# Optimization experiments

Hardware: AMD Instinct MI355X
Metric: run time of the kernel (lower is better)

## Reference

```python
import jax, jax.numpy as jnp
import numpy as np

N_NODES = 100000
N_EDGES = 3200000
F_IN, F_HID, F_OUT = 36, 8, 2
NEG_SLOPE = 0.2


def gat_layer(x, src, dst, W, a_src, a_dst, b, num_nodes):
    # Linear transform: [N, F'] 
    h = x @ W
    # Per-node attention logits (heads=1)
    alpha_s = h @ a_src  # [N]
    alpha_d = h @ a_dst  # [N]
    # Edge-wise score: leaky_relu(a_src . h_j + a_dst . h_i) for edge j->i
    e = jax.nn.leaky_relu(alpha_s[src] + alpha_d[dst], negative_slope=NEG_SLOPE)  # [E]
    # Segment softmax over incoming edges of each dst node
    m = jax.ops.segment_max(e, dst, num_segments=num_nodes)  # [N]
    ee = jnp.exp(e - m[dst])
    denom = jax.ops.segment_sum(ee, dst, num_segments=num_nodes)  # [N]
    alpha = ee / denom[dst]  # [E]
    # Scatter-aggregate messages
    out = jax.ops.segment_sum(alpha[:, None] * h[src], dst, num_segments=num_nodes)
    return out + b


def setup_inputs() -> dict:
    key = jax.random.key(0)
    ks = jax.random.split(key, 10)
    x = jax.random.normal(ks[0], (N_NODES, F_IN), dtype=jnp.float32)
    edge_index = jax.random.randint(ks[1], (2, N_EDGES), 0, N_NODES, dtype=jnp.int64)
    s1 = 1.0 / np.sqrt(F_IN)
    s2 = 1.0 / np.sqrt(F_HID)
    W1 = jax.random.uniform(ks[2], (F_IN, F_HID), jnp.float32, -s1, s1)
    a_src1 = jax.random.uniform(ks[3], (F_HID,), jnp.float32, -s2, s2)
    a_dst1 = jax.random.uniform(ks[4], (F_HID,), jnp.float32, -s2, s2)
    b1 = jnp.zeros((F_HID,), jnp.float32)
    W2 = jax.random.uniform(ks[5], (F_HID, F_OUT), jnp.float32, -s2, s2)
    so = 1.0 / np.sqrt(F_OUT)
    a_src2 = jax.random.uniform(ks[6], (F_OUT,), jnp.float32, -so, so)
    a_dst2 = jax.random.uniform(ks[7], (F_OUT,), jnp.float32, -so, so)
    b2 = jnp.zeros((F_OUT,), jnp.float32)
    return {"x": x, "edge_index": edge_index, "W1": W1, "a_src1": a_src1,
            "a_dst1": a_dst1, "b1": b1, "W2": W2, "a_src2": a_src2,
            "a_dst2": a_dst2, "b2": b2}


def reference(x, edge_index, W1, a_src1, a_dst1, b1, W2, a_src2, a_dst2, b2):
    src, dst = edge_index[0], edge_index[1]
    n = x.shape[0]
    h = jax.nn.relu(gat_layer(x, src, dst, W1, a_src1, a_dst1, b1, n))
    # dropout is identity in eval mode
    out = gat_layer(h, src, dst, W2, a_src2, a_dst2, b2, n)
    return jax.nn.log_softmax(out, axis=1)
```

## Files before the change

### kernel.cpp

```cpp
#include <hip/hip_runtime.h>
#include <hip/hip_bf16.h>

#define N_NODES 100000
#define N_EDGES 3200000
#define F_IN 36
#define F_HID 8
#define F_OUT 2
#define NEG_SLOPE 0.2f

#define SHIFT_C 10
#define NCB 98
#define CAPC 36000
#define GSHIFT 6
#define GNPB 64
#define NFINE 1568
#define CAPF 2368
#define NB_PART 512
#define CHUNK 6250
#define BP 512
#define NSLICE 16
#define BP2 256
#define BPG 256

__device__ __forceinline__ int detect_is64(const void* eidx, int* s_flag) {
    if (threadIdx.x < 64) {
        const unsigned int* p = (const unsigned int*)eidx;
        unsigned int v1 = p[2 * threadIdx.x + 1];
        unsigned int v2 = p[2 * (threadIdx.x + 64) + 1];
        unsigned long long m = __ballot(v1 != 0u || v2 != 0u);
        if (threadIdx.x == 0) *s_flag = (m == 0ull) ? 1 : 0;
    }
    __syncthreads();
    return *s_flag;
}

__global__ void part1_node1_k(const void* __restrict__ eidx, int* __restrict__ gcnt_c,
                              int* __restrict__ partC,
                              const float* __restrict__ x, const float* __restrict__ W1,
                              const float* __restrict__ aw_s, const float* __restrict__ aw_d,
                              float* __restrict__ h1, float* __restrict__ as1,
                              float* __restrict__ ad1) {
    int t = threadIdx.x;
    if (blockIdx.x >= NB_PART) {
        int n = (blockIdx.x - NB_PART) * BP + t;
        if (n >= N_NODES) return;
        float acc[F_HID];
#pragma unroll
        for (int f = 0; f < F_HID; f++) acc[f] = 0.f;
        const float4* xp = (const float4*)(x + (size_t)n * F_IN);
#pragma unroll
        for (int q = 0; q < 9; q++) {
            float4 xv = xp[q];
            const float* w = W1 + q * 4 * F_HID;
#pragma unroll
            for (int f = 0; f < F_HID; f++) {
                acc[f] += xv.x * w[0 * F_HID + f] + xv.y * w[1 * F_HID + f]
                        + xv.z * w[2 * F_HID + f] + xv.w * w[3 * F_HID + f];
            }
        }
        float s = 0.f, d = 0.f;
#pragma unroll
        for (int f = 0; f < F_HID; f++) {
            s += acc[f] * aw_s[f];
            d += acc[f] * aw_d[f];
        }
        float4* hp = (float4*)(h1 + (size_t)n * F_HID);
        hp[0] = make_float4(acc[0], acc[1], acc[2], acc[3]);
        hp[1] = make_float4(acc[4], acc[5], acc[6], acc[7]);
        as1[n] = s;
        ad1[n] = d;
        return;
    }
    __shared__ int h[NCB];
    __shared__ int s_flag;
    if (t < NCB) h[t] = 0;
    int f = detect_is64(eidx, &s_flag);
    int beg = blockIdx.x * CHUNK;
    int end = beg + CHUNK; if (end > N_EDGES) end = N_EDGES;
    if (f) {
        const long long* p = (const long long*)eidx;
        for (int i = beg + t; i < end; i += BP) atomicAdd(&h[(int)p[N_EDGES + i] >> SHIFT_C], 1);
    } else {
        const int* p = (const int*)eidx;
        for (int i = beg + t; i < end; i += BP) atomicAdd(&h[p[N_EDGES + i] >> SHIFT_C], 1);
    }
    __syncthreads();
    if (t < NCB) {
        int c = h[t];
        h[t] = c ? atomicAdd(&gcnt_c[t], c) : 0;
    }
    __syncthreads();
    if (f) {
        const long long* p = (const long long*)eidx;
        for (int i = beg + t; i < end; i += BP) {
            int s = (int)p[i];
            int d = (int)p[N_EDGES + i];
            int b = d >> SHIFT_C;
            int pos = atomicAdd(&h[b], 1);
            if (pos < CAPC) partC[b * CAPC + pos] = (s << SHIFT_C) | (d & 1023);
        }
    } else {
        const int* p = (const int*)eidx;
        for (int i = beg + t; i < end; i += BP) {
            int s = p[i];
            int d = p[N_EDGES + i];
            int b = d >> SHIFT_C;
            int pos = atomicAdd(&h[b], 1);
            if (pos < CAPC) partC[b * CAPC + pos] = (s << SHIFT_C) | (d & 1023);
        }
    }
}

__global__ void part2_k(const int* __restrict__ gcnt_c, const int* __restrict__ partC,
                        int* __restrict__ gcnt_f, int* __restrict__ fineP) {
    __shared__ int h16[16];
    __shared__ int cur16[16];
    int t = threadIdx.x;
    int cb = blockIdx.x >> 4;
    int k = blockIdx.x & 15;
    int cntc = gcnt_c[cb]; if (cntc > CAPC) cntc = CAPC;
    int sbeg = (int)((long long)k * cntc / NSLICE);
    int send = (int)((long long)(k + 1) * cntc / NSLICE);
    const int* cp = partC + (size_t)cb * CAPC;

    if (t < 16) h16[t] = 0;
    __syncthreads();
    for (int j = sbeg + t; j < send; j += BP2)
        atomicAdd(&h16[(cp[j] >> GSHIFT) & 15], 1);
    __syncthreads();
    if (t < 16) {
        int c = h16[t];
        cur16[t] = c ? atomicAdd(&gcnt_f[cb * 16 + t], c) : 0;
    }
    __syncthreads();
    for (int j = sbeg + t; j < send; j += BP2) {
        int pk = cp[j];
        int fidx = (pk >> GSHIFT) & 15;
        int pos = atomicAdd(&cur16[fidx], 1);
        if (pos < CAPF)
            fineP[(size_t)(cb * 16 + fidx) * CAPF + pos] =
                ((pk >> SHIFT_C) << GSHIFT) | (pk & (GNPB - 1));
    }
}

__global__ void gatF1_k(const int* __restrict__ gcnt_f, const int* __restrict__ fineP,
                        int* __restrict__ e_srcP, int2* __restrict__ rowinfo,
                        const float* __restrict__ as1, const float* __restrict__ ad1,
                        const float* __restrict__ h1, const float* __restrict__ b1,
                        const float* __restrict__ W2, const float* __restrict__ aw_s2,
                        const float* __restrict__ aw_d2, float4* __restrict__ P2) {
    __shared__ int eL[CAPF];
    __shared__ int hist[GNPB];
    __shared__ int nstart[GNPB];
    __shared__ int cursor[GNPB];
    __shared__ int sscan[GNPB];
    __shared__ float adl[GNPB];
    int t = threadIdx.x;
    int c = blockIdx.x;
    int nbase = c << GSHIFT;
    size_t beg = (size_t)c * CAPF;
    int cnt = gcnt_f[c]; if (cnt > CAPF) cnt = CAPF;

    if (t < GNPB) {
        hist[t] = 0;
        adl[t] = (nbase + t < N_NODES) ? ad1[nbase + t] : 0.f;
    }
    __syncthreads();
    for (int j = t; j < cnt; j += BPG)
        atomicAdd(&hist[fineP[beg + j] & (GNPB - 1)], 1);
    __syncthreads();
    if (t < GNPB) sscan[t] = hist[t];
    __syncthreads();
    for (int o = 1; o < GNPB; o <<= 1) {
        int u = (t < GNPB && t >= o) ? sscan[t - o] : 0;
        __syncthreads();
        if (t < GNPB) sscan[t] += u;
        __syncthreads();
    }
    if (t < GNPB) {
        int ex = sscan[t] - hist[t];
        nstart[t] = ex;
        cursor[t] = ex;
        int node = nbase + t;
        if (node < N_NODES) rowinfo[node] = make_int2((int)beg + ex, hist[t]);
    }
    __syncthreads();
    for (int j = t; j < cnt; j += BPG) {
        int pk = fineP[beg + j];
        int pos = atomicAdd(&cursor[pk & (GNPB - 1)], 1);
        eL[pos] = pk >> GSHIFT;
    }
    __syncthreads();
    for (int i = t; i < cnt; i += BPG) e_srcP[beg + i] = eL[i];

    int node = t >> 2;
    int lane = t & 3;
    int gnode = nbase + node;
    if (gnode >= N_NODES) return;
    int ns = nstart[node];
    int ne = ns + hist[node];
    float add = adl[node];

    float denom = 0.f;
    float acc[F_HID];
#pragma unroll
    for (int f = 0; f < F_HID; f++) acc[f] = 0.f;
    for (int i = ns + lane; i < ne; i += 4) {
        int s = eL[i];
        float e = as1[s] + add;
        e = e >= 0.f ? e : NEG_SLOPE * e;
        float ee = __expf(e);
        denom += ee;
        const float4* hp = (const float4*)(h1 + (size_t)s * F_HID);
        float4 p0 = hp[0], p1 = hp[1];
        acc[0] += ee * p0.x; acc[1] += ee * p0.y; acc[2] += ee * p0.z; acc[3] += ee * p0.w;
        acc[4] += ee * p1.x; acc[5] += ee * p1.y; acc[6] += ee * p1.z; acc[7] += ee * p1.w;
    }
#pragma unroll
    for (int o = 2; o > 0; o >>= 1) {
        denom += __shfl_xor(denom, o, 4);
#pragma unroll
        for (int f = 0; f < F_HID; f++) acc[f] += __shfl_xor(acc[f], o, 4);
    }
    if (lane == 0) {
        float inv = denom > 0.f ? 1.f / denom : 0.f;
        float o0 = 0.f, o1 = 0.f;
#pragma unroll
        for (int f = 0; f < F_HID; f++) {
            float v = acc[f] * inv + b1[f];
            v = v > 0.f ? v : 0.f;
            o0 += v * W2[f * F_OUT + 0];
            o1 += v * W2[f * F_OUT + 1];
        }
        float as2v = o0 * aw_s2[0] + o1 * aw_s2[1];
        float ad2v = o0 * aw_d2[0] + o1 * aw_d2[1];
        P2[gnode] = make_float4(as2v, o0, o1, ad2v);
    }
}

__global__ void gat2_k(const int2* __restrict__ rowinfo, const int* __restrict__ e_srcP,
                       const float4* __restrict__ P2, const float* __restrict__ b2,
                       float* __restrict__ out, int n_nodes) {
    int gid = blockIdx.x * 16 + (threadIdx.x >> 4);
    int lane = threadIdx.x & 15;
    if (gid >= n_nodes) return;
    int2 ri = rowinfo[gid];
    float add = P2[gid].w;

    float denom = 0.f, a0 = 0.f, a1 = 0.f;
    int jend = ri.x + ri.y;
    for (int j = ri.x + lane; j < jend; j += 16) {
        int s = e_srcP[j];
        float4 q = P2[s];
        float e = q.x + add;
        e = e >= 0.f ? e : NEG_SLOPE * e;
        float ee = __expf(e);
        denom += ee;
        a0 += ee * q.y;
        a1 += ee * q.z;
    }
#pragma unroll
    for (int o = 8; o > 0; o >>= 1) {
        denom += __shfl_xor(denom, o, 16);
        a0 += __shfl_xor(a0, o, 16);
        a1 += __shfl_xor(a1, o, 16);
    }

    if (lane == 0) {
        float inv = denom > 0.f ? 1.f / denom : 0.f;
        float o0 = a0 * inv + b2[0];
        float o1 = a1 * inv + b2[1];
        float M = fmaxf(o0, o1);
        float l = M + logf(__expf(o0 - M) + __expf(o1 - M));
        ((float2*)out)[gid] = make_float2(o0 - l, o1 - l);
    }
}

extern "C" void kernel_launch(void* const* d_in, const int* in_sizes, int n_in,
                              void* d_out, int out_size, void* d_ws, size_t ws_size,
                              hipStream_t stream) {
    const float* x      = (const float*)d_in[0];
    const void*  eidx   = d_in[1];
    const float* W1     = (const float*)d_in[2];
    const float* a_src1 = (const float*)d_in[3];
    const float* a_dst1 = (const float*)d_in[4];
    const float* b1     = (const float*)d_in[5];
    const float* W2     = (const float*)d_in[6];
    const float* a_src2 = (const float*)d_in[7];
    const float* a_dst2 = (const float*)d_in[8];
    const float* b2     = (const float*)d_in[9];
    float* out = (float*)d_out;

    const size_t N = N_NODES;
    const size_t SZC = (size_t)NCB * CAPC;
    const size_t SZF = (size_t)NFINE * CAPF;

    int* wsi = (int*)d_ws;
    float* wsf = (float*)d_ws;
    size_t o = 0;
    int* partC    = wsi + o;      o += SZC;
    int* fineP    = wsi + o;      o += SZF;
    int* e_srcP   = wsi + o;      o += SZF;
    int* gcnt_c   = wsi + o;      o += 128;
    int* gcnt_f   = wsi + o;      o += 1600;
    int2* rowinfo = (int2*)(wsi + o); o += 2 * N;
    float* as1    = wsf + o;      o += N;
    float* ad1    = wsf + o;      o += N;
    float* h1     = wsf + o;      o += 8 * N;
    float4* P2    = (float4*)(wsf + o); o += 4 * N;

    const int B = 256;
    const int gridG = (int)(N / 16);
    const int NODE_BLKS = (int)((N + BP - 1) / BP);

    hipMemsetAsync(gcnt_c, 0, (128 + 1600) * sizeof(int), stream);

    part1_node1_k<<<NB_PART + NODE_BLKS, BP, 0, stream>>>(
        eidx, gcnt_c, partC, x, W1, a_src1, a_dst1, h1, as1, ad1);
    part2_k<<<NCB * NSLICE, BP2, 0, stream>>>(gcnt_c, partC, gcnt_f, fineP);
    gatF1_k<<<NFINE, BPG, 0, stream>>>(gcnt_f, fineP, e_srcP, rowinfo, as1, ad1, h1, b1,
                                       W2, a_src2, a_dst2, P2);
    gat2_k<<<gridG, B, 0, stream>>>(rowinfo, e_srcP, P2, b2, out, (int)N);
}
```

Before: 186.0 us.

## Re-sort fine buckets in layer-2 kernel instead of storing CSR edge arrays

The layer-1 kernel no longer writes the sorted source-index array and per-node row info to global memory. The layer-2 kernel now reloads each fine bucket, re-sorts it in shared memory, and aggregates with 4 lanes per node, as layer 1 does. This removes one global write and read of the edge array, at the cost of repeating the shared-memory counting sort. The partition kernel's block count, chunk size and block size are also retuned.

```diff
diff --git a/kernel.cpp b/kernel.cpp
--- a/kernel.cpp
+++ b/kernel.cpp
@@ -15,9 +15,9 @@
 #define GNPB 64
 #define NFINE 1568
 #define CAPF 2368
-#define NB_PART 512
-#define CHUNK 6250
-#define BP 512
+#define NB_PART 1024
+#define CHUNK 3125
+#define BP 256
 #define NSLICE 16
 #define BP2 256
 #define BPG 256
@@ -143,8 +143,38 @@
     }
 }
 
+__device__ __forceinline__ void sort_bucket(const int* __restrict__ fineP, size_t beg, int cnt,
+                                            int* eL, int* hist, int* nstart, int* cursor,
+                                            int* sscan) {
+    int t = threadIdx.x;
+    if (t < GNPB) hist[t] = 0;
+    __syncthreads();
+    for (int j = t; j < cnt; j += BPG)
+        atomicAdd(&hist[fineP[beg + j] & (GNPB - 1)], 1);
+    __syncthreads();
+    if (t < GNPB) sscan[t] = hist[t];
+    __syncthreads();
+    for (int o = 1; o < GNPB; o <<= 1) {
+        int u = (t < GNPB && t >= o) ? sscan[t - o] : 0;
+        __syncthreads();
+        if (t < GNPB) sscan[t] += u;
+        __syncthreads();
+    }
+    if (t < GNPB) {
+        int ex = sscan[t] - hist[t];
+        nstart[t] = ex;
+        cursor[t] = ex;
+    }
+    __syncthreads();
+    for (int j = t; j < cnt; j += BPG) {
+        int pk = fineP[beg + j];
+        int pos = atomicAdd(&cursor[pk & (GNPB - 1)], 1);
+        eL[pos] = pk >> GSHIFT;
+    }
+    __syncthreads();
+}
+
 __global__ void gatF1_k(const int* __restrict__ gcnt_f, const int* __restrict__ fineP,
-                        int* __restrict__ e_srcP, int2* __restrict__ rowinfo,
                         const float* __restrict__ as1, const float* __restrict__ ad1,
                         const float* __restrict__ h1, const float* __restrict__ b1,
                         const float* __restrict__ W2, const float* __restrict__ aw_s2,
@@ -161,37 +191,8 @@
     size_t beg = (size_t)c * CAPF;
     int cnt = gcnt_f[c]; if (cnt > CAPF) cnt = CAPF;
 
-    if (t < GNPB) {
-        hist[t] = 0;
-        adl[t] = (nbase + t < N_NODES) ? ad1[nbase + t] : 0.f;
-    }
-    __syncthreads();
-    for (int j = t; j < cnt; j += BPG)
-        atomicAdd(&hist[fineP[beg + j] & (GNPB - 1)], 1);
-    __syncthreads();
-    if (t < GNPB) sscan[t] = hist[t];
-    __syncthreads();
-    for (int o = 1; o < GNPB; o <<= 1) {
-        int u = (t < GNPB && t >= o) ? sscan[t - o] : 0;
-        __syncthreads();
-        if (t < GNPB) sscan[t] += u;
-        __syncthreads();
-    }
-    if (t < GNPB) {
-        int ex = sscan[t] - hist[t];
-        nstart[t] = ex;
-        cursor[t] = ex;
-        int node = nbase + t;
-        if (node < N_NODES) rowinfo[node] = make_int2((int)beg + ex, hist[t]);
-    }
-    __syncthreads();
-    for (int j = t; j < cnt; j += BPG) {
-        int pk = fineP[beg + j];
-        int pos = atomicAdd(&cursor[pk & (GNPB - 1)], 1);
-        eL[pos] = pk >> GSHIFT;
-    }
-    __syncthreads();
-    for (int i = t; i < cnt; i += BPG) e_srcP[beg + i] = eL[i];
+    if (t < GNPB) adl[t] = (nbase + t < N_NODES) ? ad1[nbase + t] : 0.f;
+    sort_bucket(fineP, beg, cnt, eL, hist, nstart, cursor, sscan);
 
     int node = t >> 2;
     int lane = t & 3;
@@ -238,19 +239,35 @@
     }
 }
 
-__global__ void gat2_k(const int2* __restrict__ rowinfo, const int* __restrict__ e_srcP,
-                       const float4* __restrict__ P2, const float* __restrict__ b2,
-                       float* __restrict__ out, int n_nodes) {
-    int gid = blockIdx.x * 16 + (threadIdx.x >> 4);
-    int lane = threadIdx.x & 15;
-    if (gid >= n_nodes) return;
-    int2 ri = rowinfo[gid];
-    float add = P2[gid].w;
+__global__ void gatF2_k(const int* __restrict__ gcnt_f, const int* __restrict__ fineP,
+                        const float4* __restrict__ P2, const float* __restrict__ b2,
+                        float* __restrict__ out) {
+    __shared__ int eL[CAPF];
+    __shared__ int hist[GNPB];
+    __shared__ int nstart[GNPB];
+    __shared__ int cursor[GNPB];
+    __shared__ int sscan[GNPB];
+    __shared__ float adl[GNPB];
+    int t = threadIdx.x;
+    int c = blockIdx.x;
+    int nbase = c << GSHIFT;
+    size_t beg = (size_t)c * CAPF;
+    int cnt = gcnt_f[c]; if (cnt > CAPF) cnt = CAPF;
+
+    if (t < GNPB) adl[t] = (nbase + t < N_NODES) ? P2[nbase + t].w : 0.f;
+    sort_bucket(fineP, beg, cnt, eL, hist, nstart, cursor, sscan);
+
+    int node = t >> 2;
+    int lane = t & 3;
+    int gnode = nbase + node;
+    if (gnode >= N_NODES) return;
+    int ns = nstart[node];
+    int ne = ns + hist[node];
+    float add = adl[node];
 
     float denom = 0.f, a0 = 0.f, a1 = 0.f;
-    int jend = ri.x + ri.y;
-    for (int j = ri.x + lane; j < jend; j += 16) {
-        int s = e_srcP[j];
+    for (int i = ns + lane; i < ne; i += 4) {
+        int s = eL[i];
         float4 q = P2[s];
         float e = q.x + add;
         e = e >= 0.f ? e : NEG_SLOPE * e;
@@ -260,19 +277,18 @@
         a1 += ee * q.z;
     }
 #pragma unroll
-    for (int o = 8; o > 0; o >>= 1) {
-        denom += __shfl_xor(denom, o, 16);
-        a0 += __shfl_xor(a0, o, 16);
-        a1 += __shfl_xor(a1, o, 16);
-    }
-
+    for (int o = 2; o > 0; o >>= 1) {
+        denom += __shfl_xor(denom, o, 4);
+        a0 += __shfl_xor(a0, o, 4);
+        a1 += __shfl_xor(a1, o, 4);
+    }
     if (lane == 0) {
         float inv = denom > 0.f ? 1.f / denom : 0.f;
         float o0 = a0 * inv + b2[0];
         float o1 = a1 * inv + b2[1];
         float M = fmaxf(o0, o1);
         float l = M + logf(__expf(o0 - M) + __expf(o1 - M));
-        ((float2*)out)[gid] = make_float2(o0 - l, o1 - l);
+        ((float2*)out)[gnode] = make_float2(o0 - l, o1 - l);
     }
 }
 
@@ -300,17 +316,13 @@
     size_t o = 0;
     int* partC    = wsi + o;      o += SZC;
     int* fineP    = wsi + o;      o += SZF;
-    int* e_srcP   = wsi + o;      o += SZF;
     int* gcnt_c   = wsi + o;      o += 128;
     int* gcnt_f   = wsi + o;      o += 1600;
-    int2* rowinfo = (int2*)(wsi + o); o += 2 * N;
     float* as1    = wsf + o;      o += N;
     float* ad1    = wsf + o;      o += N;
     float* h1     = wsf + o;      o += 8 * N;
     float4* P2    = (float4*)(wsf + o); o += 4 * N;
 
-    const int B = 256;
-    const int gridG = (int)(N / 16);
     const int NODE_BLKS = (int)((N + BP - 1) / BP);
 
     hipMemsetAsync(gcnt_c, 0, (128 + 1600) * sizeof(int), stream);
@@ -318,7 +330,7 @@
     part1_node1_k<<<NB_PART + NODE_BLKS, BP, 0, stream>>>(
         eidx, gcnt_c, partC, x, W1, a_src1, a_dst1, h1, as1, ad1);
     part2_k<<<NCB * NSLICE, BP2, 0, stream>>>(gcnt_c, partC, gcnt_f, fineP);
-    gatF1_k<<<NFINE, BPG, 0, stream>>>(gcnt_f, fineP, e_srcP, rowinfo, as1, ad1, h1, b1,
+    gatF1_k<<<NFINE, BPG, 0, stream>>>(gcnt_f, fineP, as1, ad1, h1, b1,
                                        W2, a_src2, a_dst2, P2);
-    gat2_k<<<gridG, B, 0, stream>>>(rowinfo, e_srcP, P2, b2, out, (int)N);
-}
+    gatF2_k<<<NFINE, BPG, 0, stream>>>(gcnt_f, fineP, P2, b2, out);
+}
```

New measurement: 205.4 us. 1.1x slower.
